# Kernel tuning notes

Hardware: AMD Instinct MI355X
Metric: run time of the kernel (lower is better)

The kernel has to match this reference:

```python
import jax, jax.numpy as jnp
import numpy as np

B, F_SIZE, DIM = 2048, 32, 64
LAYER_SIZES = (128, 128)


def setup_inputs() -> dict:
    key = jax.random.key(0)
    k1, k2, k3 = jax.random.split(key, 3)
    inputs = jax.random.normal(k1, (B, F_SIZE, DIM), dtype=jnp.float32)
    # Conv1d(kernel=1) weights: (out_channels, in_channels)
    W0 = jax.random.normal(k2, (128, F_SIZE * F_SIZE), dtype=jnp.float32) * 0.03
    b0 = jnp.zeros((128,), dtype=jnp.float32)
    # split_half -> field_nums[1] = 64 -> in_channels = 64 * 32 = 2048
    W1 = jax.random.normal(k3, (128, 64 * F_SIZE), dtype=jnp.float32) * 0.03
    b1 = jnp.zeros((128,), dtype=jnp.float32)
    return {"inputs": inputs, "W0": W0, "b0": b0, "W1": W1, "b1": b1}


def _cin_forward(inputs, Ws, bs):
    batch, _, dim = inputs.shape
    x0 = inputs
    h = inputs
    finals = []
    n_layers = len(Ws)
    for i in range(n_layers):
        H = h.shape[1]
        M = x0.shape[1]
        # outer-product interaction: (b, H, M, d) -> (b, H*M, d)
        z = jnp.einsum('bhd,bmd->bhmd', h, x0).reshape(batch, H * M, dim)
        # 1x1 conv == per-position channel matmul
        out = jnp.einsum('bcd,oc->bod', z, Ws[i]) + bs[i][None, :, None]
        out = jax.nn.relu(out)
        size = Ws[i].shape[0]
        if i != n_layers - 1:
            # split_half: first half feeds next layer, second half is output
            h = out[:, : size // 2, :]
            finals.append(out[:, size // 2 :, :])
        else:
            finals.append(out)
    result = jnp.concatenate(finals, axis=1)  # (b, 64 + 128, d)
    return jnp.sum(result, axis=-1)           # (b, 192)


def reference(inputs, W0, b0, W1, b1):
    return _cin_forward(inputs, (W0, W1), (b0, b1))
```

## Files before the change

### kernel.cpp

```cpp
#include <hip/hip_runtime.h>
#include <hip/hip_bf16.h>


#define BATCH 2048
#define FSZ   32
#define DIM   64
#define K0    1024
#define K1    2048
#define OUTC  192

#define W0_FRAGS 16384
#define W1_FRAGS 32768
#define W0_ELEMS (128 * K0)

typedef _Float16 v8h __attribute__((ext_vector_type(8)));
typedef float    v4f __attribute__((ext_vector_type(4)));

#define XT_PITCH 40
#define XD_PITCH 66
#define HD_PITCH 66

__global__ void convert_w_kernel(const float* __restrict__ W0,
                                 const float* __restrict__ W1,
                                 _Float16* __restrict__ wsw) {
    int t = blockIdx.x * blockDim.x + threadIdx.x;
    if (t < W0_FRAGS) {
        int ks = t >> 9, s = (t >> 6) & 7, lane = t & 63;
        int row = s * 16 + (lane & 15);
        int k0  = ks * 32 + (lane >> 4) * 8;
        const float* src = W0 + (size_t)row * K0 + k0;
        _Float16* dst = wsw + (size_t)t * 8;
        #pragma unroll
        for (int j = 0; j < 8; ++j) dst[j] = (_Float16)src[j];
    } else if (t < W0_FRAGS + W1_FRAGS) {
        int u = t - W0_FRAGS;
        int ks = u >> 9, s = (u >> 6) & 7, lane = u & 63;
        int row = s * 16 + (lane & 15);
        int k0  = ks * 32 + (lane >> 4) * 8;
        const float* src = W1 + (size_t)row * K1 + k0;
        _Float16* dst = wsw + W0_ELEMS + (size_t)u * 8;
        #pragma unroll
        for (int j = 0; j < 8; ++j) dst[j] = (_Float16)src[j];
    }
}

__global__ __launch_bounds__(256, 4) void cin_kernel(
    const float* __restrict__ X,
    const float* __restrict__ b0,
    const float* __restrict__ b1,
    const _Float16* __restrict__ Wsw,
    float* __restrict__ out)
{
    __shared__ _Float16 xT[DIM * XT_PITCH];
    __shared__ _Float16 xD[FSZ * XD_PITCH];
    __shared__ _Float16 h1D[64 * HD_PITCH];

    const int b    = blockIdx.x;
    const int tid  = threadIdx.x;
    const int wave = tid >> 6;
    const int lane = tid & 63;
    const int quad = lane >> 4;
    const int col  = lane & 15;

    const float* xb = X + (size_t)b * (FSZ * DIM);
    #pragma unroll
    for (int i = tid; i < FSZ * DIM; i += 256) {
        int m = i >> 6, d = i & 63;
        _Float16 v = (_Float16)xb[i];
        xT[d * XT_PITCH + m] = v;
        xD[m * XD_PITCH + d] = v;
    }
    __syncthreads();

    v8h xv8[4];
    int dd[4];
    #pragma unroll
    for (int t = 0; t < 4; ++t) {
        dd[t] = 16 * t + col;
        xv8[t] = *(const v8h*)(&xT[dd[t] * XT_PITCH + quad * 8]);
    }

    v4f acc[2][4];
    #pragma unroll
    for (int r = 0; r < 2; ++r)
        #pragma unroll
        for (int t = 0; t < 4; ++t) acc[r][t] = (v4f)0.0f;

    {
        const _Float16* Wk = Wsw + (size_t)wave * 2 * 512 + (size_t)lane * 8;
        #pragma unroll 4
        for (int ks = 0; ks < 32; ++ks) {
            v8h a0 = *(const v8h*)(Wk);
            v8h a1 = *(const v8h*)(Wk + 512);
            Wk += 4096;
            #pragma unroll
            for (int t = 0; t < 4; ++t) {
                _Float16 s = xD[ks * XD_PITCH + dd[t]];
                v8h s8 = {s, s, s, s, s, s, s, s};
                v8h bfr = s8 * xv8[t];
                acc[0][t] = __builtin_amdgcn_mfma_f32_16x16x32_f16(a0, bfr, acc[0][t], 0, 0, 0);
                acc[1][t] = __builtin_amdgcn_mfma_f32_16x16x32_f16(a1, bfr, acc[1][t], 0, 0, 0);
            }
        }
    }

    #pragma unroll
    for (int r = 0; r < 2; ++r) {
        const int obase = wave * 32 + r * 16 + quad * 4;
        if (obase < 64) {
            #pragma unroll
            for (int reg = 0; reg < 4; ++reg) {
                float bias = b0[obase + reg];
                #pragma unroll
                for (int t = 0; t < 4; ++t) {
                    float v = acc[r][t][reg] + bias;
                    v = v > 0.0f ? v : 0.0f;
                    h1D[(obase + reg) * HD_PITCH + dd[t]] = (_Float16)v;
                }
            }
        } else {
            #pragma unroll
            for (int reg = 0; reg < 4; ++reg) {
                float bias = b0[obase + reg];
                float s = 0.0f;
                #pragma unroll
                for (int t = 0; t < 4; ++t) {
                    float v = acc[r][t][reg] + bias;
                    s += (v > 0.0f ? v : 0.0f);
                }
                s += __shfl_xor(s, 1);
                s += __shfl_xor(s, 2);
                s += __shfl_xor(s, 4);
                s += __shfl_xor(s, 8);
                if (col == 0) out[(size_t)b * OUTC + (obase + reg - 64)] = s;
            }
        }
    }
    __syncthreads();

    #pragma unroll
    for (int r = 0; r < 2; ++r)
        #pragma unroll
        for (int t = 0; t < 4; ++t) acc[r][t] = (v4f)0.0f;

    {
        const _Float16* Wk = Wsw + W0_ELEMS + (size_t)wave * 2 * 512 + (size_t)lane * 8;
        #pragma unroll 4
        for (int ks = 0; ks < 64; ++ks) {
            v8h a0 = *(const v8h*)(Wk);
            v8h a1 = *(const v8h*)(Wk + 512);
            Wk += 4096;
            #pragma unroll
            for (int t = 0; t < 4; ++t) {
                _Float16 s = h1D[ks * HD_PITCH + dd[t]];
                v8h s8 = {s, s, s, s, s, s, s, s};
                v8h bfr = s8 * xv8[t];
                acc[0][t] = __builtin_amdgcn_mfma_f32_16x16x32_f16(a0, bfr, acc[0][t], 0, 0, 0);
                acc[1][t] = __builtin_amdgcn_mfma_f32_16x16x32_f16(a1, bfr, acc[1][t], 0, 0, 0);
            }
        }
    }

    #pragma unroll
    for (int r = 0; r < 2; ++r) {
        const int obase = wave * 32 + r * 16 + quad * 4;
        #pragma unroll
        for (int reg = 0; reg < 4; ++reg) {
            float bias = b1[obase + reg];
            float s = 0.0f;
            #pragma unroll
            for (int t = 0; t < 4; ++t) {
                float v = acc[r][t][reg] + bias;
                s += (v > 0.0f ? v : 0.0f);
            }
            s += __shfl_xor(s, 1);
            s += __shfl_xor(s, 2);
            s += __shfl_xor(s, 4);
            s += __shfl_xor(s, 8);
            if (col == 0) out[(size_t)b * OUTC + 64 + obase + reg] = s;
        }
    }
}

extern "C" void kernel_launch(void* const* d_in, const int* in_sizes, int n_in,
                              void* d_out, int out_size, void* d_ws, size_t ws_size,
                              hipStream_t stream) {
    const float* X  = (const float*)d_in[0];
    const float* W0 = (const float*)d_in[1];
    const float* b0 = (const float*)d_in[2];
    const float* W1 = (const float*)d_in[3];
    const float* b1 = (const float*)d_in[4];
    float* out = (float*)d_out;
    _Float16* wsw = (_Float16*)d_ws;

    convert_w_kernel<<<(W0_FRAGS + W1_FRAGS + 255) / 256, 256, 0, stream>>>(W0, W1, wsw);
    cin_kernel<<<BATCH, 256, 0, stream>>>(X, b0, b1, wsw, out);
}
```

Before: 158.7 us.

## Switch CIN GEMMs to 32x32x16 MFMA with matching weight fragment layout

```diff
diff --git a/kernel.cpp b/kernel.cpp
--- a/kernel.cpp
+++ b/kernel.cpp
@@ -1,5 +1,4 @@
 #include <hip/hip_runtime.h>
-#include <hip/hip_bf16.h>
 
 
 #define BATCH 2048
@@ -9,12 +8,13 @@
 #define K1    2048
 #define OUTC  192
 
-#define W0_FRAGS 16384
-#define W1_FRAGS 32768
 #define W0_ELEMS (128 * K0)
+#define W1_ELEMS (128 * K1)
+#define TOT_ELEMS (W0_ELEMS + W1_ELEMS)
+#define CVT_THREADS (TOT_ELEMS / 4)
 
-typedef _Float16 v8h __attribute__((ext_vector_type(8)));
-typedef float    v4f __attribute__((ext_vector_type(4)));
+typedef _Float16 v8h  __attribute__((ext_vector_type(8)));
+typedef float    v16f __attribute__((ext_vector_type(16)));
 
 #define XT_PITCH 40
 #define XD_PITCH 66
@@ -24,24 +24,27 @@
                                  const float* __restrict__ W1,
                                  _Float16* __restrict__ wsw) {
     int t = blockIdx.x * blockDim.x + threadIdx.x;
-    if (t < W0_FRAGS) {
-        int ks = t >> 9, s = (t >> 6) & 7, lane = t & 63;
-        int row = s * 16 + (lane & 15);
-        int k0  = ks * 32 + (lane >> 4) * 8;
-        const float* src = W0 + (size_t)row * K0 + k0;
-        _Float16* dst = wsw + (size_t)t * 8;
-        #pragma unroll
-        for (int j = 0; j < 8; ++j) dst[j] = (_Float16)src[j];
-    } else if (t < W0_FRAGS + W1_FRAGS) {
-        int u = t - W0_FRAGS;
-        int ks = u >> 9, s = (u >> 6) & 7, lane = u & 63;
-        int row = s * 16 + (lane & 15);
-        int k0  = ks * 32 + (lane >> 4) * 8;
-        const float* src = W1 + (size_t)row * K1 + k0;
-        _Float16* dst = wsw + W0_ELEMS + (size_t)u * 8;
-        #pragma unroll
-        for (int j = 0; j < 8; ++j) dst[j] = (_Float16)src[j];
+    if (t >= CVT_THREADS) return;
+    int e = t * 4;
+    const float* src;
+    if (e < W0_ELEMS) {
+        int f = e >> 3, j0 = e & 7;
+        int ks = f >> 8, ob = (f >> 6) & 3, lane = f & 63;
+        src = W0 + (size_t)(ob * 32 + (lane & 31)) * K0
+                 + ks * 16 + (lane >> 5) * 8 + j0;
+    } else {
+        int u = e - W0_ELEMS;
+        int f = u >> 3, j0 = u & 7;
+        int ks = f >> 8, ob = (f >> 6) & 3, lane = f & 63;
+        src = W1 + (size_t)(ob * 32 + (lane & 31)) * K1
+                 + ks * 16 + (lane >> 5) * 8 + j0;
     }
+    float4 v = *(const float4*)src;
+    _Float16* dst = wsw + e;
+    dst[0] = (_Float16)v.x;
+    dst[1] = (_Float16)v.y;
+    dst[2] = (_Float16)v.z;
+    dst[3] = (_Float16)v.w;
 }
 
 __global__ __launch_bounds__(256, 4) void cin_kernel(
@@ -59,8 +62,8 @@
     const int tid  = threadIdx.x;
     const int wave = tid >> 6;
     const int lane = tid & 63;
-    const int quad = lane >> 4;
-    const int col  = lane & 15;
+    const int half = lane >> 5;
+    const int d0   = lane & 31;
 
     const float* xb = X + (size_t)b * (FSZ * DIM);
     #pragma unroll
@@ -72,113 +75,94 @@
     }
     __syncthreads();
 
-    v8h xv8[4];
-    int dd[4];
+    v8h xh[2][2];
     #pragma unroll
-    for (int t = 0; t < 4; ++t) {
-        dd[t] = 16 * t + col;
-        xv8[t] = *(const v8h*)(&xT[dd[t] * XT_PITCH + quad * 8]);
+    for (int db = 0; db < 2; ++db)
+        #pragma unroll
+        for (int p = 0; p < 2; ++p)
+            xh[db][p] = *(const v8h*)(&xT[(db * 32 + d0) * XT_PITCH + p * 16 + half * 8]);
+
+    v16f acc0 = (v16f)0.0f;
+    v16f acc1 = (v16f)0.0f;
+
+    {
+        const _Float16* Wk = Wsw + (size_t)(wave * 64 + lane) * 8;
+        #pragma unroll 4
+        for (int ks = 0; ks < 64; ++ks) {
+            v8h a = *(const v8h*)(Wk + (size_t)ks * 2048);
+            const int hr = ks >> 1;
+            _Float16 s0 = xD[hr * XD_PITCH + d0];
+            _Float16 s1 = xD[hr * XD_PITCH + 32 + d0];
+            v8h s08 = {s0, s0, s0, s0, s0, s0, s0, s0};
+            v8h s18 = {s1, s1, s1, s1, s1, s1, s1, s1};
+            v8h bf0 = s08 * xh[0][ks & 1];
+            v8h bf1 = s18 * xh[1][ks & 1];
+            acc0 = __builtin_amdgcn_mfma_f32_32x32x16_f16(a, bf0, acc0, 0, 0, 0);
+            acc1 = __builtin_amdgcn_mfma_f32_32x32x16_f16(a, bf1, acc1, 0, 0, 0);
+        }
     }
 
-    v4f acc[2][4];
-    #pragma unroll
-    for (int r = 0; r < 2; ++r)
+    if (wave < 2) {
         #pragma unroll
-        for (int t = 0; t < 4; ++t) acc[r][t] = (v4f)0.0f;
+        for (int reg = 0; reg < 16; ++reg) {
+            const int o = wave * 32 + (reg & 3) + 8 * (reg >> 2) + 4 * half;
+            const float bias = b0[o];
+            float v0 = acc0[reg] + bias; v0 = v0 > 0.0f ? v0 : 0.0f;
+            float v1 = acc1[reg] + bias; v1 = v1 > 0.0f ? v1 : 0.0f;
+            h1D[o * HD_PITCH + d0]      = (_Float16)v0;
+            h1D[o * HD_PITCH + 32 + d0] = (_Float16)v1;
+        }
+    } else {
+        #pragma unroll
+        for (int reg = 0; reg < 16; ++reg) {
+            const int o = wave * 32 + (reg & 3) + 8 * (reg >> 2) + 4 * half;
+            const float bias = b0[o];
+            float v0 = acc0[reg] + bias; v0 = v0 > 0.0f ? v0 : 0.0f;
+            float v1 = acc1[reg] + bias; v1 = v1 > 0.0f ? v1 : 0.0f;
+            float s = v0 + v1;
+            s += __shfl_xor(s, 1);
+            s += __shfl_xor(s, 2);
+            s += __shfl_xor(s, 4);
+            s += __shfl_xor(s, 8);
+            s += __shfl_xor(s, 16);
+            if (d0 == 0) out[(size_t)b * OUTC + (o - 64)] = s;
+        }
+    }
+    __syncthreads();
+
+    acc0 = (v16f)0.0f;
+    acc1 = (v16f)0.0f;
 
     {
-        const _Float16* Wk = Wsw + (size_t)wave * 2 * 512 + (size_t)lane * 8;
+        const _Float16* Wk = Wsw + W0_ELEMS + (size_t)(wave * 64 + lane) * 8;
         #pragma unroll 4
-        for (int ks = 0; ks < 32; ++ks) {
-            v8h a0 = *(const v8h*)(Wk);
-            v8h a1 = *(const v8h*)(Wk + 512);
-            Wk += 4096;
-            #pragma unroll
-            for (int t = 0; t < 4; ++t) {
-                _Float16 s = xD[ks * XD_PITCH + dd[t]];
-                v8h s8 = {s, s, s, s, s, s, s, s};
-                v8h bfr = s8 * xv8[t];
-                acc[0][t] = __builtin_amdgcn_mfma_f32_16x16x32_f16(a0, bfr, acc[0][t], 0, 0, 0);
-                acc[1][t] = __builtin_amdgcn_mfma_f32_16x16x32_f16(a1, bfr, acc[1][t], 0, 0, 0);
-            }
+        for (int ks = 0; ks < 128; ++ks) {
+            v8h a = *(const v8h*)(Wk + (size_t)ks * 2048);
+            const int hr = ks >> 1;
+            _Float16 s0 = h1D[hr * HD_PITCH + d0];
+            _Float16 s1 = h1D[hr * HD_PITCH + 32 + d0];
+            v8h s08 = {s0, s0, s0, s0, s0, s0, s0, s0};
+            v8h s18 = {s1, s1, s1, s1, s1, s1, s1, s1};
+            v8h bf0 = s08 * xh[0][ks & 1];
+            v8h bf1 = s18 * xh[1][ks & 1];
+            acc0 = __builtin_amdgcn_mfma_f32_32x32x16_f16(a, bf0, acc0, 0, 0, 0);
+            acc1 = __builtin_amdgcn_mfma_f32_32x32x16_f16(a, bf1, acc1, 0, 0, 0);
         }
     }
 
     #pragma unroll
-    for (int r = 0; r < 2; ++r) {
-        const int obase = wave * 32 + r * 16 + quad * 4;
-        if (obase < 64) {
-            #pragma unroll
-            for (int reg = 0; reg < 4; ++reg) {
-                float bias = b0[obase + reg];
-                #pragma unroll
-                for (int t = 0; t < 4; ++t) {
-                    float v = acc[r][t][reg] + bias;
-                    v = v > 0.0f ? v : 0.0f;
-                    h1D[(obase + reg) * HD_PITCH + dd[t]] = (_Float16)v;
-                }
-            }
-        } else {
-            #pragma unroll
-            for (int reg = 0; reg < 4; ++reg) {
-                float bias = b0[obase + reg];
-                float s = 0.0f;
-                #pragma unroll
-                for (int t = 0; t < 4; ++t) {
-                    float v = acc[r][t][reg] + bias;
-                    s += (v > 0.0f ? v : 0.0f);
-                }
-                s += __shfl_xor(s, 1);
-                s += __shfl_xor(s, 2);
-                s += __shfl_xor(s, 4);
-                s += __shfl_xor(s, 8);
-                if (col == 0) out[(size_t)b * OUTC + (obase + reg - 64)] = s;
-            }
-        }
-    }
-    __syncthreads();
-
-    #pragma unroll
-    for (int r = 0; r < 2; ++r)
-        #pragma unroll
-        for (int t = 0; t < 4; ++t) acc[r][t] = (v4f)0.0f;
-
-    {
-        const _Float16* Wk = Wsw + W0_ELEMS + (size_t)wave * 2 * 512 + (size_t)lane * 8;
-        #pragma unroll 4
-        for (int ks = 0; ks < 64; ++ks) {
-            v8h a0 = *(const v8h*)(Wk);
-            v8h a1 = *(const v8h*)(Wk + 512);
-            Wk += 4096;
-            #pragma unroll
-            for (int t = 0; t < 4; ++t) {
-                _Float16 s = h1D[ks * HD_PITCH + dd[t]];
-                v8h s8 = {s, s, s, s, s, s, s, s};
-                v8h bfr = s8 * xv8[t];
-                acc[0][t] = __builtin_amdgcn_mfma_f32_16x16x32_f16(a0, bfr, acc[0][t], 0, 0, 0);
-                acc[1][t] = __builtin_amdgcn_mfma_f32_16x16x32_f16(a1, bfr, acc[1][t], 0, 0, 0);
-            }
-        }
-    }
-
-    #pragma unroll
-    for (int r = 0; r < 2; ++r) {
-        const int obase = wave * 32 + r * 16 + quad * 4;
-        #pragma unroll
-        for (int reg = 0; reg < 4; ++reg) {
-            float bias = b1[obase + reg];
-            float s = 0.0f;
-            #pragma unroll
-            for (int t = 0; t < 4; ++t) {
-                float v = acc[r][t][reg] + bias;
-                s += (v > 0.0f ? v : 0.0f);
-            }
-            s += __shfl_xor(s, 1);
-            s += __shfl_xor(s, 2);
-            s += __shfl_xor(s, 4);
-            s += __shfl_xor(s, 8);
-            if (col == 0) out[(size_t)b * OUTC + 64 + obase + reg] = s;
-        }
+    for (int reg = 0; reg < 16; ++reg) {
+        const int o = wave * 32 + (reg & 3) + 8 * (reg >> 2) + 4 * half;
+        const float bias = b1[o];
+        float v0 = acc0[reg] + bias; v0 = v0 > 0.0f ? v0 : 0.0f;
+        float v1 = acc1[reg] + bias; v1 = v1 > 0.0f ? v1 : 0.0f;
+        float s = v0 + v1;
+        s += __shfl_xor(s, 1);
+        s += __shfl_xor(s, 2);
+        s += __shfl_xor(s, 4);
+        s += __shfl_xor(s, 8);
+        s += __shfl_xor(s, 16);
+        if (d0 == 0) out[(size_t)b * OUTC + 64 + o] = s;
     }
 }
 
@@ -193,6 +177,6 @@
     float* out = (float*)d_out;
     _Float16* wsw = (_Float16*)d_ws;
 
-    convert_w_kernel<<<(W0_FRAGS + W1_FRAGS + 255) / 256, 256, 0, stream>>>(W0, W1, wsw);
+    convert_w_kernel<<<(CVT_THREADS + 255) / 256, 256, 0, stream>>>(W0, W1, wsw);
     cin_kernel<<<BATCH, 256, 0, stream>>>(X, b0, b1, wsw, out);
 }
```

Result: slower. 179.6 us (+13.2%).

## Process two batch rows per block with four-fragment weight reuse per wave

Applied to the files above, without the earlier changes.

```diff
diff --git a/kernel.cpp b/kernel.cpp
--- a/kernel.cpp
+++ b/kernel.cpp
@@ -1,5 +1,4 @@
 #include <hip/hip_runtime.h>
-#include <hip/hip_bf16.h>
 
 
 #define BATCH 2048
@@ -9,9 +8,10 @@
 #define K1    2048
 #define OUTC  192
 
-#define W0_FRAGS 16384
-#define W1_FRAGS 32768
 #define W0_ELEMS (128 * K0)
+#define W1_ELEMS (128 * K1)
+#define TOT_ELEMS (W0_ELEMS + W1_ELEMS)
+#define CVT_THREADS (TOT_ELEMS / 4)
 
 typedef _Float16 v8h __attribute__((ext_vector_type(8)));
 typedef float    v4f __attribute__((ext_vector_type(4)));
@@ -24,24 +24,27 @@
                                  const float* __restrict__ W1,
                                  _Float16* __restrict__ wsw) {
     int t = blockIdx.x * blockDim.x + threadIdx.x;
-    if (t < W0_FRAGS) {
-        int ks = t >> 9, s = (t >> 6) & 7, lane = t & 63;
-        int row = s * 16 + (lane & 15);
-        int k0  = ks * 32 + (lane >> 4) * 8;
-        const float* src = W0 + (size_t)row * K0 + k0;
-        _Float16* dst = wsw + (size_t)t * 8;
-        #pragma unroll
-        for (int j = 0; j < 8; ++j) dst[j] = (_Float16)src[j];
-    } else if (t < W0_FRAGS + W1_FRAGS) {
-        int u = t - W0_FRAGS;
-        int ks = u >> 9, s = (u >> 6) & 7, lane = u & 63;
-        int row = s * 16 + (lane & 15);
-        int k0  = ks * 32 + (lane >> 4) * 8;
-        const float* src = W1 + (size_t)row * K1 + k0;
-        _Float16* dst = wsw + W0_ELEMS + (size_t)u * 8;
-        #pragma unroll
-        for (int j = 0; j < 8; ++j) dst[j] = (_Float16)src[j];
-    }
+    if (t >= CVT_THREADS) return;
+    int e = t * 4;
+    const float* src;
+    _Float16* dst;
+    if (e < W0_ELEMS) {
+        int j0 = e & 7, lane = (e >> 3) & 63, s = (e >> 9) & 7, ks = e >> 12;
+        src = W0 + (size_t)(s * 16 + (lane & 15)) * K0
+                 + ks * 32 + (lane >> 4) * 8 + j0;
+        dst = wsw + e;
+    } else {
+        int u = e - W0_ELEMS;
+        int j0 = u & 7, lane = (u >> 3) & 63, s = (u >> 9) & 7, ks = u >> 12;
+        src = W1 + (size_t)(s * 16 + (lane & 15)) * K1
+                 + ks * 32 + (lane >> 4) * 8 + j0;
+        dst = wsw + W0_ELEMS + u;
+    }
+    float4 v = *(const float4*)src;
+    dst[0] = (_Float16)v.x;
+    dst[1] = (_Float16)v.y;
+    dst[2] = (_Float16)v.z;
+    dst[3] = (_Float16)v.w;
 }
 
 __global__ __launch_bounds__(256, 4) void cin_kernel(
@@ -51,24 +54,34 @@
     const _Float16* __restrict__ Wsw,
     float* __restrict__ out)
 {
-    __shared__ _Float16 xT[DIM * XT_PITCH];
-    __shared__ _Float16 xD[FSZ * XD_PITCH];
-    __shared__ _Float16 h1D[64 * HD_PITCH];
-
-    const int b    = blockIdx.x;
+    __shared__ _Float16 xT[2][DIM * XT_PITCH];
+    __shared__ _Float16 xD[2][FSZ * XD_PITCH];
+    __shared__ _Float16 h1D[2][64 * HD_PITCH];
+
+    const int b0i  = blockIdx.x * 2;
     const int tid  = threadIdx.x;
     const int wave = tid >> 6;
     const int lane = tid & 63;
+    const int p    = wave & 1;
+    const int rh   = wave >> 1;
     const int quad = lane >> 4;
     const int col  = lane & 15;
 
-    const float* xb = X + (size_t)b * (FSZ * DIM);
-    #pragma unroll
-    for (int i = tid; i < FSZ * DIM; i += 256) {
-        int m = i >> 6, d = i & 63;
-        _Float16 v = (_Float16)xb[i];
-        xT[d * XT_PITCH + m] = v;
-        xD[m * XD_PITCH + d] = v;
+    #pragma unroll
+    for (int i = tid; i < 2 * FSZ * DIM / 4; i += 256) {
+        int pp = i >> 9, r4 = i & 511;
+        float4 v = *(const float4*)(X + (size_t)(b0i + pp) * (FSZ * DIM) + r4 * 4);
+        int m = (r4 * 4) >> 6, d = (r4 * 4) & 63;
+        _Float16 f0 = (_Float16)v.x, f1 = (_Float16)v.y,
+                 f2 = (_Float16)v.z, f3 = (_Float16)v.w;
+        xT[pp][(d + 0) * XT_PITCH + m] = f0;
+        xT[pp][(d + 1) * XT_PITCH + m] = f1;
+        xT[pp][(d + 2) * XT_PITCH + m] = f2;
+        xT[pp][(d + 3) * XT_PITCH + m] = f3;
+        xD[pp][m * XD_PITCH + d + 0] = f0;
+        xD[pp][m * XD_PITCH + d + 1] = f1;
+        xD[pp][m * XD_PITCH + d + 2] = f2;
+        xD[pp][m * XD_PITCH + d + 3] = f3;
     }
     __syncthreads();
 
@@ -77,107 +90,119 @@
     #pragma unroll
     for (int t = 0; t < 4; ++t) {
         dd[t] = 16 * t + col;
-        xv8[t] = *(const v8h*)(&xT[dd[t] * XT_PITCH + quad * 8]);
-    }
-
-    v4f acc[2][4];
-    #pragma unroll
-    for (int r = 0; r < 2; ++r)
-        #pragma unroll
-        for (int t = 0; t < 4; ++t) acc[r][t] = (v4f)0.0f;
+        xv8[t] = *(const v8h*)(&xT[p][dd[t] * XT_PITCH + quad * 8]);
+    }
+
+    v4f acc[4][4];
+    #pragma unroll
+    for (int f = 0; f < 4; ++f)
+        #pragma unroll
+        for (int t = 0; t < 4; ++t) acc[f][t] = (v4f)0.0f;
 
     {
-        const _Float16* Wk = Wsw + (size_t)wave * 2 * 512 + (size_t)lane * 8;
-        #pragma unroll 4
+        const _Float16* Wk = Wsw + (size_t)(rh * 4) * 512 + (size_t)lane * 8;
+        #pragma unroll 2
         for (int ks = 0; ks < 32; ++ks) {
             v8h a0 = *(const v8h*)(Wk);
             v8h a1 = *(const v8h*)(Wk + 512);
+            v8h a2 = *(const v8h*)(Wk + 1024);
+            v8h a3 = *(const v8h*)(Wk + 1536);
             Wk += 4096;
             #pragma unroll
             for (int t = 0; t < 4; ++t) {
-                _Float16 s = xD[ks * XD_PITCH + dd[t]];
+                _Float16 s = xD[p][ks * XD_PITCH + dd[t]];
                 v8h s8 = {s, s, s, s, s, s, s, s};
                 v8h bfr = s8 * xv8[t];
                 acc[0][t] = __builtin_amdgcn_mfma_f32_16x16x32_f16(a0, bfr, acc[0][t], 0, 0, 0);
                 acc[1][t] = __builtin_amdgcn_mfma_f32_16x16x32_f16(a1, bfr, acc[1][t], 0, 0, 0);
-            }
-        }
-    }
-
-    #pragma unroll
-    for (int r = 0; r < 2; ++r) {
-        const int obase = wave * 32 + r * 16 + quad * 4;
-        if (obase < 64) {
+                acc[2][t] = __builtin_amdgcn_mfma_f32_16x16x32_f16(a2, bfr, acc[2][t], 0, 0, 0);
+                acc[3][t] = __builtin_amdgcn_mfma_f32_16x16x32_f16(a3, bfr, acc[3][t], 0, 0, 0);
+            }
+        }
+    }
+
+    if (rh == 0) {
+        #pragma unroll
+        for (int f = 0; f < 4; ++f) {
             #pragma unroll
             for (int reg = 0; reg < 4; ++reg) {
-                float bias = b0[obase + reg];
+                const int o = f * 16 + quad * 4 + reg;
+                const float bias = b0[o];
                 #pragma unroll
                 for (int t = 0; t < 4; ++t) {
-                    float v = acc[r][t][reg] + bias;
+                    float v = acc[f][t][reg] + bias;
                     v = v > 0.0f ? v : 0.0f;
-                    h1D[(obase + reg) * HD_PITCH + dd[t]] = (_Float16)v;
+                    h1D[p][o * HD_PITCH + dd[t]] = (_Float16)v;
                 }
             }
-        } else {
+        }
+    } else {
+        #pragma unroll
+        for (int f = 0; f < 4; ++f) {
             #pragma unroll
             for (int reg = 0; reg < 4; ++reg) {
-                float bias = b0[obase + reg];
+                const int o = 64 + f * 16 + quad * 4 + reg;
+                const float bias = b0[o];
                 float s = 0.0f;
                 #pragma unroll
                 for (int t = 0; t < 4; ++t) {
-                    float v = acc[r][t][reg] + bias;
+                    float v = acc[f][t][reg] + bias;
                     s += (v > 0.0f ? v : 0.0f);
                 }
                 s += __shfl_xor(s, 1);
                 s += __shfl_xor(s, 2);
                 s += __shfl_xor(s, 4);
                 s += __shfl_xor(s, 8);
-                if (col == 0) out[(size_t)b * OUTC + (obase + reg - 64)] = s;
+                if (col == 0) out[(size_t)(b0i + p) * OUTC + (o - 64)] = s;
             }
         }
     }
     __syncthreads();
 
     #pragma unroll
-    for (int r = 0; r < 2; ++r)
-        #pragma unroll
-        for (int t = 0; t < 4; ++t) acc[r][t] = (v4f)0.0f;
+    for (int f = 0; f < 4; ++f)
+        #pragma unroll
+        for (int t = 0; t < 4; ++t) acc[f][t] = (v4f)0.0f;
 
     {
-        const _Float16* Wk = Wsw + W0_ELEMS + (size_t)wave * 2 * 512 + (size_t)lane * 8;
-        #pragma unroll 4
+        const _Float16* Wk = Wsw + W0_ELEMS + (size_t)(rh * 4) * 512 + (size_t)lane * 8;
+        #pragma unroll 2
         for (int ks = 0; ks < 64; ++ks) {
             v8h a0 = *(const v8h*)(Wk);
             v8h a1 = *(const v8h*)(Wk + 512);
+            v8h a2 = *(const v8h*)(Wk + 1024);
+            v8h a3 = *(const v8h*)(Wk + 1536);
             Wk += 4096;
             #pragma unroll
             for (int t = 0; t < 4; ++t) {
-                _Float16 s = h1D[ks * HD_PITCH + dd[t]];
+                _Float16 s = h1D[p][ks * HD_PITCH + dd[t]];
                 v8h s8 = {s, s, s, s, s, s, s, s};
                 v8h bfr = s8 * xv8[t];
                 acc[0][t] = __builtin_amdgcn_mfma_f32_16x16x32_f16(a0, bfr, acc[0][t], 0, 0, 0);
                 acc[1][t] = __builtin_amdgcn_mfma_f32_16x16x32_f16(a1, bfr, acc[1][t], 0, 0, 0);
-            }
-        }
-    }
-
-    #pragma unroll
-    for (int r = 0; r < 2; ++r) {
-        const int obase = wave * 32 + r * 16 + quad * 4;
+                acc[2][t] = __builtin_amdgcn_mfma_f32_16x16x32_f16(a2, bfr, acc[2][t], 0, 0, 0);
+                acc[3][t] = __builtin_amdgcn_mfma_f32_16x16x32_f16(a3, bfr, acc[3][t], 0, 0, 0);
+            }
+        }
+    }
+
+    #pragma unroll
+    for (int f = 0; f < 4; ++f) {
         #pragma unroll
         for (int reg = 0; reg < 4; ++reg) {
-            float bias = b1[obase + reg];
+            const int o = rh * 64 + f * 16 + quad * 4 + reg;
+            const float bias = b1[o];
             float s = 0.0f;
             #pragma unroll
             for (int t = 0; t < 4; ++t) {
-                float v = acc[r][t][reg] + bias;
+                float v = acc[f][t][reg] + bias;
                 s += (v > 0.0f ? v : 0.0f);
             }
             s += __shfl_xor(s, 1);
             s += __shfl_xor(s, 2);
             s += __shfl_xor(s, 4);
             s += __shfl_xor(s, 8);
-            if (col == 0) out[(size_t)b * OUTC + 64 + obase + reg] = s;
+            if (col == 0) out[(size_t)(b0i + p) * OUTC + 64 + o] = s;
         }
     }
 }
@@ -193,6 +218,6 @@
     float* out = (float*)d_out;
     _Float16* wsw = (_Float16*)d_ws;
 
-    convert_w_kernel<<<(W0_FRAGS + W1_FRAGS + 255) / 256, 256, 0, stream>>>(W0, W1, wsw);
-    cin_kernel<<<BATCH, 256, 0, stream>>>(X, b0, b1, wsw, out);
+    convert_w_kernel<<<(CVT_THREADS + 255) / 256, 256, 0, stream>>>(W0, W1, wsw);
+    cin_kernel<<<BATCH / 2, 256, 0, stream>>>(X, b0, b1, wsw, out);
 }
```

Result: faster. 150.1 us (-5.4%).
